# Optimization experiments

Hardware: AMD Instinct MI355X
Metric: run time of the kernel (lower is better)

Reference implementation:

```python
import jax, jax.numpy as jnp
import numpy as np

B, L, D, T, NL = 64, 512, 512, 5000, 2


def setup_inputs() -> dict:
    key = jax.random.key(0)
    k1, k2, k3, k4 = jax.random.split(key, 4)
    enc_output = jax.random.normal(k1, (B, L, D), dtype=jnp.float32)
    # stands in for the row/col-normalized tag co-occurrence matrix (values in [0, 0.01])
    ui_adj = jax.random.uniform(k2, (T, T), dtype=jnp.float32) * 0.01
    # one GCN weight matrix per layer in the layer_stack
    Ws = jax.random.normal(k3, (NL, D, D), dtype=jnp.float32) / np.sqrt(D).astype(np.float32)
    # event ids are 1-indexed in the original (it indexes with e - 1)
    event_type = jax.random.randint(k4, (B, L), 1, T + 1, dtype=jnp.int64)
    slf_attn_mask = jnp.zeros((B, L, L), dtype=bool)
    non_pad_mask = jnp.ones((B, L), dtype=bool)
    return {"enc_output": enc_output, "ui_adj": ui_adj, "Ws": Ws,
            "event_type": event_type, "slf_attn_mask": slf_attn_mask,
            "non_pad_mask": non_pad_mask}


def reference(enc_output, ui_adj, Ws, event_type, slf_attn_mask, non_pad_mask):
    # --- batched per-sample adjacency gather (replaces the Python loop) ---
    idx = event_type - 1                                   # [B, L] 0-indexed
    sub = ui_adj[idx[:, :, None], idx[:, None, :]]         # [B, L, L] = ui_adj[e-1,:][:, e-1]
    diag = ui_adj[idx, idx]                                # [B, L]   = ui_adj[e-1, e-1]
    adj = sub + diag[:, None, :]                           # vector broadcasts across rows, as in torch
    # --- GNN layer stack (hGCN layer ~ relu(A @ X @ W)) ---
    x = enc_output
    for l in range(Ws.shape[0]):                           # small fixed n_layers loop
        x = jax.nn.relu(jnp.einsum('bij,bjd->bid', adj, x) @ Ws[l])
    # --- mean pool over sequence ---
    return x.mean(axis=1)                                  # [B, D]
```

## Files before the change

### kernel.cpp

```cpp
#include <hip/hip_runtime.h>

typedef unsigned short u16;
typedef unsigned int u32;
typedef __bf16 bf16x8 __attribute__((ext_vector_type(8)));
typedef float f32x4 __attribute__((ext_vector_type(4)));
typedef int i32x4 __attribute__((ext_vector_type(4)));
typedef u32 u32x2 __attribute__((ext_vector_type(2)));
typedef u32 u32x4 __attribute__((ext_vector_type(4)));

#define T_ 5000
#define CAP 96

__device__ __forceinline__ u16 f2bf(float f) {
  u32 u = __float_as_uint(f);
  u += 0x7fffu + ((u >> 16) & 1u);
  return (u16)(u >> 16);
}

__device__ __forceinline__ void gload_lds16(const u16* g, u16* l) {
  __builtin_amdgcn_global_load_lds(
      (__attribute__((address_space(1))) void*)(u16*)g,
      (__attribute__((address_space(3))) void*)l, 16, 0, 0);
}

__device__ __forceinline__ u32 lds_off(const void* p) {
  return (u32)(uintptr_t)(__attribute__((address_space(3))) const void*)p;
}

__device__ __forceinline__ u32 swz(int row, int kb) {
  return (u32)((row >> 1) * 128 +
               ((((row & 1) << 6) | kb) ^ (((row >> 1) & 7) << 4)));
}

__global__ void prep_k(const float* __restrict__ src, u16* __restrict__ dst,
                       int* __restrict__ cnt) {
  __shared__ float tile[32][33];
  const int tx = threadIdx.x, ty = threadIdx.y;
  const int a0 = blockIdx.x * 32;
  const int b0 = blockIdx.y * 32;
  const size_t zoff = (size_t)blockIdx.z * (512 * 512);
  const float* s = src + zoff;
  u16* d = dst + zoff;
#pragma unroll
  for (int r = 0; r < 4; ++r)
    tile[ty + r * 8][tx] = s[(size_t)(a0 + ty + r * 8) * 512 + b0 + tx];
  const int gid = ((blockIdx.z * 16 + blockIdx.y) * 16 + blockIdx.x) * 256 + ty * 32 + tx;
  if (gid < 5008) cnt[gid] = 0;
  __syncthreads();
#pragma unroll
  for (int r = 0; r < 4; ++r)
    d[(size_t)(b0 + ty + r * 8) * 512 + a0 + tx] = f2bf(tile[tx][ty + r * 8]);
}

__global__ void fill_k(const int* __restrict__ ev, const float* __restrict__ ui,
                       int2* __restrict__ cd, int* __restrict__ cnt,
                       int* __restrict__ list, int* __restrict__ ovf) {
  const int t = blockIdx.x * 256 + threadIdx.x;
  const int r = ev[t] - 1;
  int2 v;
  v.x = r;
  v.y = __float_as_int(ui[(size_t)r * (T_ + 1)]);
  cd[t] = v;
  const int pos = atomicAdd(&cnt[r], 1);
  if (pos < CAP) list[r * CAP + pos] = t;
  else { const int o = atomicAdd(&cnt[5000], 1); ovf[o] = t; }
}

__global__ __launch_bounds__(256)
void grow_gather(const float* __restrict__ ui, const int2* __restrict__ cd,
                 const int* __restrict__ cnt, const int* __restrict__ list,
                 const int* __restrict__ ovf, u16* __restrict__ adj) {
  __shared__ float row[5000];
  __shared__ int lst[CAP];
  const int r = blockIdx.x;
  int c = cnt[r];
  if (c > CAP) c = CAP;
  const int j = threadIdx.x * 2;
  if (c > 0) {
    const float* __restrict__ src = ui + (size_t)r * T_;
    for (int t = threadIdx.x; t < 1250; t += 256)
      *(float4*)&row[t * 4] = *(const float4*)&src[t * 4];
    if (threadIdx.x < c) lst[threadIdx.x] = list[r * CAP + threadIdx.x];
    __syncthreads();
    int q = 0;
    for (; q + 4 <= c; q += 4) {
      const int t0 = lst[q], t1 = lst[q + 1], t2 = lst[q + 2], t3 = lst[q + 3];
      const int4 p0 = *(const int4*)&cd[((t0 >> 9) << 9) + j];
      const int4 p1 = *(const int4*)&cd[((t1 >> 9) << 9) + j];
      const int4 p2 = *(const int4*)&cd[((t2 >> 9) << 9) + j];
      const int4 p3 = *(const int4*)&cd[((t3 >> 9) << 9) + j];
      const u32 k0 = (u32)f2bf(row[p0.x] + __int_as_float(p0.y)) |
                     ((u32)f2bf(row[p0.z] + __int_as_float(p0.w)) << 16);
      const u32 k1 = (u32)f2bf(row[p1.x] + __int_as_float(p1.y)) |
                     ((u32)f2bf(row[p1.z] + __int_as_float(p1.w)) << 16);
      const u32 k2 = (u32)f2bf(row[p2.x] + __int_as_float(p2.y)) |
                     ((u32)f2bf(row[p2.z] + __int_as_float(p2.w)) << 16);
      const u32 k3 = (u32)f2bf(row[p3.x] + __int_as_float(p3.y)) |
                     ((u32)f2bf(row[p3.z] + __int_as_float(p3.w)) << 16);
      *(u32*)&adj[(size_t)t0 * 512 + j] = k0;
      *(u32*)&adj[(size_t)t1 * 512 + j] = k1;
      *(u32*)&adj[(size_t)t2 * 512 + j] = k2;
      *(u32*)&adj[(size_t)t3 * 512 + j] = k3;
    }
    for (; q < c; ++q) {
      const int t0 = lst[q];
      const int4 p0 = *(const int4*)&cd[((t0 >> 9) << 9) + j];
      const u32 k0 = (u32)f2bf(row[p0.x] + __int_as_float(p0.y)) |
                     ((u32)f2bf(row[p0.z] + __int_as_float(p0.w)) << 16);
      *(u32*)&adj[(size_t)t0 * 512 + j] = k0;
    }
  }
  if (r < 8) {
    const int n = cnt[5000];
    for (int q = r; q < n; q += 8) {
      const int t = ovf[q];
      const long rr = (long)cd[t].x;
      const float* __restrict__ rp = ui + rr * (long)T_;
      const int4 p = *(const int4*)&cd[((t >> 9) << 9) + j];
      const u32 pk = (u32)f2bf(rp[p.x] + __int_as_float(p.y)) |
                     ((u32)f2bf(rp[p.z] + __int_as_float(p.w)) << 16);
      *(u32*)&adj[(size_t)t * 512 + j] = pk;
    }
  }
}

template <int MODE, int BSRC>
__global__ __launch_bounds__(512, 2)
void gemm256(const u16* __restrict__ A, const void* __restrict__ Bv,
             u16* __restrict__ C, size_t strideA, size_t strideB, size_t strideC,
             float* __restrict__ P) {
  extern __shared__ u16 smem[];
  const int tid = threadIdx.x;
  const int lane = tid & 63;
  const int w = tid >> 6;
  const int wm = w >> 2, wn = w & 3;
  const int chunk = gridDim.x >> 3;
  const int wg = blockIdx.x;
  const int mapped = (wg & 7) * chunk + (wg >> 3);
  const int batch = mapped >> 2;
  const int tm = (mapped >> 1) & 1, tn = mapped & 1;
  const int m0 = tm << 8, n0 = tn << 8;
  const int r0base = (MODE == 3) ? n0 : m0;
  const int r1base = (MODE == 3) ? m0 : n0;
  const u16* __restrict__ Ab = A + (size_t)batch * strideA;

  const u16* gA[2];
  u32 ldA[2];
#pragma unroll
  for (int r = 0; r < 2; ++r) {
    const int c = r * 512 + tid;
    const int L = c * 16;
    const int pp = L >> 7;
    const int off = (L & 127) ^ ((pp & 7) << 4);
    const int m = pp * 2 + (off >> 6);
    const int kb = off & 63;
    gA[r] = Ab + (size_t)(r0base + m) * 512 + (kb >> 1);
    ldA[r] = (u32)((r * 512 + w * 64) * 8);
  }

  const u16* gB[2] = {nullptr, nullptr};
  u32 ldB[2] = {0, 0};
  if (BSRC == 0) {
    const u16* __restrict__ Bb = (const u16*)Bv + (size_t)batch * strideB;
#pragma unroll
    for (int r = 0; r < 2; ++r) {
      const int c = r * 512 + tid;
      const int L = c * 16;
      const int pp = L >> 7;
      const int off = (L & 127) ^ ((pp & 7) << 4);
      const int m = pp * 2 + (off >> 6);
      const int kb = off & 63;
      gB[r] = Bb + (size_t)(r1base + m) * 512 + (kb >> 1);
      ldB[r] = (u32)(32768 + (r * 512 + w * 64) * 8);
    }
  }

  const int dp = tid & 127;
  const int lq = tid >> 7;
  unsigned long long encB = 0;
  u32 boff0 = 0;
  u32x2 bs0[8], bs1[8];
  if (BSRC == 1) {
    encB = (unsigned long long)(uintptr_t)((const float*)Bv + (size_t)batch * strideB);
    boff0 = (u32)(((lq * 8) * 512 + r1base + dp * 2) * 4);
  }

#define BLOAD(t, S)                                                          \
  {                                                                          \
    const u32 ob = boff0 + (u32)(t) * 65536u;                                \
    _Pragma("unroll") for (int i = 0; i < 8; ++i)                            \
        asm volatile("global_load_dwordx2 %0, %1, %2"                        \
                     : "=v"(S[i])                                            \
                     : "v"(ob + (u32)i * 2048u), "s"(encB));                 \
  }

#define CONVERT_B(S)                                                         \
  {                                                                          \
    u32 wrd0[4], wrd1[4];                                                    \
    _Pragma("unroll") for (int jj = 0; jj < 4; ++jj) {                       \
      asm("v_cvt_pk_bf16_f32 %0, %1, %2"                                     \
          : "=v"(wrd0[jj]) : "v"(S[2 * jj].x), "v"(S[2 * jj + 1].x));        \
      asm("v_cvt_pk_bf16_f32 %0, %1, %2"                                     \
          : "=v"(wrd1[jj]) : "v"(S[2 * jj].y), "v"(S[2 * jj + 1].y));        \
    }                                                                        \
    const u32 by0 = (u32)dp * 128u + ((((u32)lq * 16u)) ^ (((u32)dp & 7u) << 4)); \
    const u32 by1 = (u32)dp * 128u + ((64u | ((u32)lq * 16u)) ^ (((u32)dp & 7u) << 4)); \
    u32x4 v0, v1;                                                            \
    v0.x = wrd0[0]; v0.y = wrd0[1]; v0.z = wrd0[2]; v0.w = wrd0[3];          \
    v1.x = wrd1[0]; v1.y = wrd1[1]; v1.z = wrd1[2]; v1.w = wrd1[3];          \
    *(u32x4*)((char*)smem + 65536 + by0) = v0;                               \
    *(u32x4*)((char*)smem + 65536 + by1) = v1;                               \
  }

  const int lr = lane & 15;
  const int kbB = (lane >> 4) << 4;
  u32 fOff8[8], fOff4[4];
#pragma unroll
  for (int m = 0; m < 8; ++m) fOff8[m] = swz(wm * 128 + m * 16 + lr, kbB);
#pragma unroll
  for (int n = 0; n < 4; ++n) fOff4[n] = swz(wn * 64 + n * 16 + lr, kbB);
  const u32 ldsBase = lds_off(smem);

  f32x4 acc[8][4] = {};

  auto stageA = [&](int t) {
    const u32 bo = (u32)(t & 3) * 8192;
#pragma unroll
    for (int r = 0; r < 2; ++r) gload_lds16(gA[r] + t * 32, smem + bo + ldA[r]);
  };
  auto stageB0 = [&](int t) {
    const u32 bo = (u32)(t & 3) * 8192;
#pragma unroll
    for (int r = 0; r < 2; ++r) gload_lds16(gB[r] + t * 32, smem + bo + ldB[r]);
  };

  if (BSRC == 0) {
    stageA(0); stageB0(0); stageA(1); stageB0(1); stageA(2); stageB0(2);
  } else {
    stageA(0); stageA(1); stageA(2);
    BLOAD(0, bs0); BLOAD(1, bs1);
  }

#pragma unroll
  for (int t = 0; t < 16; ++t) {
    if (BSRC == 0) {
      if (t <= 13)      asm volatile("s_waitcnt vmcnt(8)" ::: "memory");
      else if (t == 14) asm volatile("s_waitcnt vmcnt(4)" ::: "memory");
      else              asm volatile("s_waitcnt vmcnt(0)" ::: "memory");
      __builtin_amdgcn_sched_barrier(0);
      if (t + 3 < 16) { stageA(t + 3); stageB0(t + 3); }
      asm volatile("" ::: "memory");
      __builtin_amdgcn_s_barrier();
      asm volatile("" ::: "memory");
    } else {
      if (t == 0)              asm volatile("s_waitcnt vmcnt(8)" ::: "memory");
      else if (t <= 13)        asm volatile("s_waitcnt vmcnt(10)" ::: "memory");
      else if (t == 14)        asm volatile("s_waitcnt vmcnt(8)" ::: "memory");
      else                     asm volatile("s_waitcnt vmcnt(0)" ::: "memory");
      __builtin_amdgcn_sched_barrier(0);
      if (t & 1) { CONVERT_B(bs1); } else { CONVERT_B(bs0); }
      if (t + 3 < 16) stageA(t + 3);
      if (t + 2 < 16) { if (t & 1) { BLOAD(t + 2, bs1); } else { BLOAD(t + 2, bs0); } }
      asm volatile("s_waitcnt lgkmcnt(0)" ::: "memory");
      __builtin_amdgcn_s_barrier();
      asm volatile("" ::: "memory");
    }

    const u32 c0 = ldsBase + (u32)(t & 3) * 16384;
    const u32 c1 = ldsBase + 65536u + (BSRC == 0 ? (u32)(t & 3) * 16384 : 0u);
    const u32 base8 = (MODE == 3) ? c1 : c0;
    const u32 base4 = (MODE == 3) ? c0 : c1;
    i32x4 araw[8], braw[4];

#pragma unroll
    for (int n = 0; n < 4; ++n)
      asm volatile("ds_read_b128 %0, %1" : "=v"(braw[n]) : "v"(base4 + fOff4[n]));
#pragma unroll
    for (int m = 0; m < 4; ++m)
      asm volatile("ds_read_b128 %0, %1" : "=v"(araw[m]) : "v"(base8 + fOff8[m]));
    asm volatile("s_waitcnt lgkmcnt(0)" ::: "memory");
    __builtin_amdgcn_sched_barrier(0);
    __builtin_amdgcn_s_setprio(1);
#pragma unroll
    for (int m = 0; m < 4; ++m)
#pragma unroll
      for (int n = 0; n < 4; ++n)
        acc[m][n] = __builtin_amdgcn_mfma_f32_16x16x32_bf16(
            __builtin_bit_cast(bf16x8, araw[m]),
            __builtin_bit_cast(bf16x8, braw[n]), acc[m][n], 0, 0, 0);
    __builtin_amdgcn_s_setprio(0);
    asm volatile("" ::: "memory");
    __builtin_amdgcn_s_barrier();
    asm volatile("" ::: "memory");

#pragma unroll
    for (int m = 4; m < 8; ++m)
      asm volatile("ds_read_b128 %0, %1" : "=v"(araw[m]) : "v"(base8 + fOff8[m]));
    asm volatile("s_waitcnt lgkmcnt(0)" ::: "memory");
    __builtin_amdgcn_sched_barrier(0);
    __builtin_amdgcn_s_setprio(1);
#pragma unroll
    for (int m = 4; m < 8; ++m)
#pragma unroll
      for (int n = 0; n < 4; ++n)
        acc[m][n] = __builtin_amdgcn_mfma_f32_16x16x32_bf16(
            __builtin_bit_cast(bf16x8, araw[m]),
            __builtin_bit_cast(bf16x8, braw[n]), acc[m][n], 0, 0, 0);
    __builtin_amdgcn_s_setprio(0);
    asm volatile("" ::: "memory");
    __builtin_amdgcn_s_barrier();
    __builtin_amdgcn_sched_barrier(0);
  }
#undef BLOAD
#undef CONVERT_B

  u16* Cb = C + (size_t)batch * strideC;
  if (MODE == 1) {
#pragma unroll
    for (int m = 0; m < 8; ++m) {
      const int i = m0 + wm * 128 + m * 16 + (lane >> 4) * 4;
#pragma unroll
      for (int n = 0; n < 4; ++n) {
        const int d = n0 + wn * 64 + n * 16 + (lane & 15);
        const f32x4 v = acc[m][n];
        uint2 p;
        p.x = (u32)f2bf(fmaxf(v[0], 0.f)) | ((u32)f2bf(fmaxf(v[1], 0.f)) << 16);
        p.y = (u32)f2bf(fmaxf(v[2], 0.f)) | ((u32)f2bf(fmaxf(v[3], 0.f)) << 16);
        *(uint2*)&Cb[(size_t)d * 512 + i] = p;
      }
    }
  } else if (MODE == 2) {
    const int slot = tm * 2 + wm;
#pragma unroll
    for (int n = 0; n < 4; ++n) {
      float s = 0.f;
#pragma unroll
      for (int m = 0; m < 8; ++m) {
        const f32x4 v = acc[m][n];
#pragma unroll
        for (int j = 0; j < 4; ++j) s += fmaxf(v[j], 0.f);
      }
      s += __shfl_xor(s, 16);
      s += __shfl_xor(s, 32);
      if ((lane >> 4) == 0) {
        const int d = n0 + wn * 64 + n * 16 + lane;
        P[((size_t)batch * 4 + slot) * 512 + d] = s;
      }
    }
  } else {
#pragma unroll
    for (int m = 0; m < 8; ++m) {
      const int dd = m0 + wm * 128 + m * 16 + (lane >> 4) * 4;
#pragma unroll
      for (int n = 0; n < 4; ++n) {
        const int ii = n0 + wn * 64 + n * 16 + (lane & 15);
        const f32x4 v = acc[m][n];
        uint2 p;
        p.x = (u32)f2bf(v[0]) | ((u32)f2bf(v[1]) << 16);
        p.y = (u32)f2bf(v[2]) | ((u32)f2bf(v[3]) << 16);
        *(uint2*)&Cb[(size_t)ii * 512 + dd] = p;
      }
    }
  }
}

__global__ void reduce_mean(const float* __restrict__ P, float* __restrict__ out) {
  const int t = blockIdx.x * 256 + threadIdx.x;
  const int b = t >> 9, d = t & 511;
  float s = 0.f;
#pragma unroll
  for (int q = 0; q < 4; ++q) s += P[((size_t)b * 4 + q) * 512 + d];
  out[t] = s * (1.0f / 512.0f);
}

extern "C" void kernel_launch(void* const* d_in, const int* in_sizes, int n_in,
                              void* d_out, int out_size, void* d_ws, size_t ws_size,
                              hipStream_t stream) {
  const float* enc = (const float*)d_in[0];
  const float* ui  = (const float*)d_in[1];
  const float* Ws  = (const float*)d_in[2];
  const int*   ev  = (const int*)d_in[3];
  float* out = (float*)d_out;

  char* ws = (char*)d_ws;
  const size_t SLAB = (size_t)64 * 512 * 512 * 2;
  u16* adj  = (u16*)(ws);
  u16* tbuf = (u16*)(ws + SLAB);
  u16* xb   = (u16*)(ws + 2 * SLAB);
  char* p = ws + 3 * SLAB;
  u16* wst  = (u16*)p;  p += (size_t)2 * 512 * 512 * 2;
  int2* cd  = (int2*)p; p += (size_t)32768 * 8;
  int* cnt  = (int*)p;  p += 5008 * 4;
  int* list = (int*)p;  p += (size_t)5000 * CAP * 4;
  int* ovf  = (int*)p;  p += (size_t)32768 * 4;
  float* P  = (float*)p;

  const size_t PS = (size_t)512 * 512;
  const size_t SMEM0 = 131072;
  const size_t SMEM1 = 81920;
  (void)hipFuncSetAttribute(reinterpret_cast<const void*>(gemm256<3, 1>),
                            hipFuncAttributeMaxDynamicSharedMemorySize, (int)SMEM1);
  (void)hipFuncSetAttribute(reinterpret_cast<const void*>(gemm256<1, 0>),
                            hipFuncAttributeMaxDynamicSharedMemorySize, (int)SMEM0);
  (void)hipFuncSetAttribute(reinterpret_cast<const void*>(gemm256<3, 0>),
                            hipFuncAttributeMaxDynamicSharedMemorySize, (int)SMEM0);
  (void)hipFuncSetAttribute(reinterpret_cast<const void*>(gemm256<2, 0>),
                            hipFuncAttributeMaxDynamicSharedMemorySize, (int)SMEM0);

  prep_k<<<dim3(16, 16, 2), dim3(32, 8), 0, stream>>>(Ws, wst, cnt);
  fill_k<<<128, 256, 0, stream>>>(ev, ui, cd, cnt, list, ovf);
  grow_gather<<<5000, 256, 0, stream>>>(ui, cd, cnt, list, ovf, adj);
  gemm256<3, 1><<<256, 512, SMEM1, stream>>>(adj, enc, tbuf, PS, PS, PS, nullptr);
  gemm256<1, 0><<<256, 512, SMEM0, stream>>>(tbuf, wst, xb, PS, 0, PS, nullptr);
  gemm256<3, 0><<<256, 512, SMEM0, stream>>>(adj, xb, tbuf, PS, PS, PS, nullptr);
  gemm256<2, 0><<<256, 512, SMEM0, stream>>>(tbuf, wst + PS, nullptr, PS, 0, 0, P);
  reduce_mean<<<128, 256, 0, stream>>>(P, out);
}
```

Measured before the change: 143.7 us.

## Add 8-phase ping-pong GEMM kernel with 64-wide K tiles for bf16 GEMMs

```diff
diff --git a/kernel.cpp b/kernel.cpp
--- a/kernel.cpp
+++ b/kernel.cpp
@@ -158,23 +158,6 @@
     ldA[r] = (u32)((r * 512 + w * 64) * 8);
   }
 
-  const u16* gB[2] = {nullptr, nullptr};
-  u32 ldB[2] = {0, 0};
-  if (BSRC == 0) {
-    const u16* __restrict__ Bb = (const u16*)Bv + (size_t)batch * strideB;
-#pragma unroll
-    for (int r = 0; r < 2; ++r) {
-      const int c = r * 512 + tid;
-      const int L = c * 16;
-      const int pp = L >> 7;
-      const int off = (L & 127) ^ ((pp & 7) << 4);
-      const int m = pp * 2 + (off >> 6);
-      const int kb = off & 63;
-      gB[r] = Bb + (size_t)(r1base + m) * 512 + (kb >> 1);
-      ldB[r] = (u32)(32768 + (r * 512 + w * 64) * 8);
-    }
-  }
-
   const int dp = tid & 127;
   const int lq = tid >> 7;
   unsigned long long encB = 0;
@@ -228,61 +211,41 @@
 #pragma unroll
     for (int r = 0; r < 2; ++r) gload_lds16(gA[r] + t * 32, smem + bo + ldA[r]);
   };
-  auto stageB0 = [&](int t) {
-    const u32 bo = (u32)(t & 3) * 8192;
-#pragma unroll
-    for (int r = 0; r < 2; ++r) gload_lds16(gB[r] + t * 32, smem + bo + ldB[r]);
-  };
-
-  if (BSRC == 0) {
-    stageA(0); stageB0(0); stageA(1); stageB0(1); stageA(2); stageB0(2);
-  } else {
-    stageA(0); stageA(1); stageA(2);
-    BLOAD(0, bs0); BLOAD(1, bs1);
-  }
+
+  stageA(0); stageA(1); stageA(2);
+  BLOAD(0, bs0); BLOAD(1, bs1);
 
 #pragma unroll
   for (int t = 0; t < 16; ++t) {
-    if (BSRC == 0) {
-      if (t <= 13)      asm volatile("s_waitcnt vmcnt(8)" ::: "memory");
-      else if (t == 14) asm volatile("s_waitcnt vmcnt(4)" ::: "memory");
-      else              asm volatile("s_waitcnt vmcnt(0)" ::: "memory");
-      __builtin_amdgcn_sched_barrier(0);
-      if (t + 3 < 16) { stageA(t + 3); stageB0(t + 3); }
-      asm volatile("" ::: "memory");
-      __builtin_amdgcn_s_barrier();
-      asm volatile("" ::: "memory");
-    } else {
-      if (t == 0)              asm volatile("s_waitcnt vmcnt(8)" ::: "memory");
-      else if (t <= 13)        asm volatile("s_waitcnt vmcnt(10)" ::: "memory");
-      else if (t == 14)        asm volatile("s_waitcnt vmcnt(8)" ::: "memory");
-      else                     asm volatile("s_waitcnt vmcnt(0)" ::: "memory");
-      __builtin_amdgcn_sched_barrier(0);
-      if (t & 1) { CONVERT_B(bs1); } else { CONVERT_B(bs0); }
-      if (t + 3 < 16) stageA(t + 3);
-      if (t + 2 < 16) { if (t & 1) { BLOAD(t + 2, bs1); } else { BLOAD(t + 2, bs0); } }
-      asm volatile("s_waitcnt lgkmcnt(0)" ::: "memory");
-      __builtin_amdgcn_s_barrier();
-      asm volatile("" ::: "memory");
-    }
+    if (t == 0)              asm volatile("s_waitcnt vmcnt(8)" ::: "memory");
+    else if (t <= 13)        asm volatile("s_waitcnt vmcnt(10)" ::: "memory");
+    else if (t == 14)        asm volatile("s_waitcnt vmcnt(8)" ::: "memory");
+    else                     asm volatile("s_waitcnt vmcnt(0)" ::: "memory");
+    __builtin_amdgcn_sched_barrier(0);
+    if (t & 1) { CONVERT_B(bs1); } else { CONVERT_B(bs0); }
+    if (t + 3 < 16) stageA(t + 3);
+    if (t + 2 < 16) { if (t & 1) { BLOAD(t + 2, bs1); } else { BLOAD(t + 2, bs0); } }
+    asm volatile("s_waitcnt lgkmcnt(0)" ::: "memory");
+    __builtin_amdgcn_s_barrier();
+    asm volatile("" ::: "memory");
 
     const u32 c0 = ldsBase + (u32)(t & 3) * 16384;
-    const u32 c1 = ldsBase + 65536u + (BSRC == 0 ? (u32)(t & 3) * 16384 : 0u);
+    const u32 c1 = ldsBase + 65536u;
     const u32 base8 = (MODE == 3) ? c1 : c0;
     const u32 base4 = (MODE == 3) ? c0 : c1;
     i32x4 araw[8], braw[4];
-
+#pragma unroll
+    for (int m = 0; m < 8; ++m)
+      asm volatile("ds_read_b128 %0, %1" : "=v"(araw[m]) : "v"(base8 + fOff8[m]));
 #pragma unroll
     for (int n = 0; n < 4; ++n)
       asm volatile("ds_read_b128 %0, %1" : "=v"(braw[n]) : "v"(base4 + fOff4[n]));
-#pragma unroll
-    for (int m = 0; m < 4; ++m)
-      asm volatile("ds_read_b128 %0, %1" : "=v"(araw[m]) : "v"(base8 + fOff8[m]));
     asm volatile("s_waitcnt lgkmcnt(0)" ::: "memory");
     __builtin_amdgcn_sched_barrier(0);
+
     __builtin_amdgcn_s_setprio(1);
 #pragma unroll
-    for (int m = 0; m < 4; ++m)
+    for (int m = 0; m < 8; ++m)
 #pragma unroll
       for (int n = 0; n < 4; ++n)
         acc[m][n] = __builtin_amdgcn_mfma_f32_16x16x32_bf16(
@@ -291,28 +254,213 @@
     __builtin_amdgcn_s_setprio(0);
     asm volatile("" ::: "memory");
     __builtin_amdgcn_s_barrier();
-    asm volatile("" ::: "memory");
-
-#pragma unroll
-    for (int m = 4; m < 8; ++m)
-      asm volatile("ds_read_b128 %0, %1" : "=v"(araw[m]) : "v"(base8 + fOff8[m]));
-    asm volatile("s_waitcnt lgkmcnt(0)" ::: "memory");
-    __builtin_amdgcn_sched_barrier(0);
-    __builtin_amdgcn_s_setprio(1);
-#pragma unroll
-    for (int m = 4; m < 8; ++m)
-#pragma unroll
-      for (int n = 0; n < 4; ++n)
-        acc[m][n] = __builtin_amdgcn_mfma_f32_16x16x32_bf16(
-            __builtin_bit_cast(bf16x8, araw[m]),
-            __builtin_bit_cast(bf16x8, braw[n]), acc[m][n], 0, 0, 0);
-    __builtin_amdgcn_s_setprio(0);
-    asm volatile("" ::: "memory");
-    __builtin_amdgcn_s_barrier();
     __builtin_amdgcn_sched_barrier(0);
   }
 #undef BLOAD
 #undef CONVERT_B
+
+  u16* Cb = C + (size_t)batch * strideC;
+#pragma unroll
+  for (int m = 0; m < 8; ++m) {
+    const int dd = m0 + wm * 128 + m * 16 + (lane >> 4) * 4;
+#pragma unroll
+    for (int n = 0; n < 4; ++n) {
+      const int ii = n0 + wn * 64 + n * 16 + (lane & 15);
+      const f32x4 v = acc[m][n];
+      uint2 p;
+      p.x = (u32)f2bf(v[0]) | ((u32)f2bf(v[1]) << 16);
+      p.y = (u32)f2bf(v[2]) | ((u32)f2bf(v[3]) << 16);
+      *(uint2*)&Cb[(size_t)ii * 512 + dd] = p;
+    }
+  }
+  (void)P;
+}
+
+template <int MODE>
+__global__ __launch_bounds__(512, 2)
+void gemm8p(const u16* __restrict__ A, const u16* __restrict__ Bm,
+            u16* __restrict__ C, size_t strideA, size_t strideB, size_t strideC,
+            float* __restrict__ P) {
+  extern __shared__ u16 smem[];
+  const int tid = threadIdx.x;
+  const int lane = tid & 63;
+  const int w = tid >> 6;
+  const int wm = w >> 2, wn = w & 3;
+  const int chunk = gridDim.x >> 3;
+  const int wg = blockIdx.x;
+  const int mapped = (wg & 7) * chunk + (wg >> 3);
+  const int batch = mapped >> 2;
+  const int tm = (mapped >> 1) & 1, tn = mapped & 1;
+  const int m0 = tm << 8, n0 = tn << 8;
+  const int r0base = (MODE == 3) ? n0 : m0;
+  const int r1base = (MODE == 3) ? m0 : n0;
+  const u16* __restrict__ Ab = A + (size_t)batch * strideA;
+  const u16* __restrict__ Bb = Bm + (size_t)batch * strideB;
+
+  const u16* gR0[2];
+  const u16* gR1[2];
+  u32 ldR0[2], ldR1[2];
+#pragma unroll
+  for (int rr = 0; rr < 2; ++rr) {
+    const int cc = rr * 512 + tid;
+    const int row = cc >> 3;
+    const int kb = ((cc & 7) * 16) ^ ((row & 7) << 4);
+    gR0[rr] = Ab + (size_t)(r0base + row) * 512 + (kb >> 1);
+    gR1[rr] = Bb + (size_t)(r1base + row) * 512 + (kb >> 1);
+    ldR0[rr] = (u32)((rr * 512 + w * 64) * 8);
+    ldR1[rr] = (u32)(32768 + (rr * 512 + w * 64) * 8);
+  }
+
+  const int lr = lane & 15;
+  const int hi16 = (lane >> 4) * 16;
+  u32 o8[8][2], o4[4][2];
+#pragma unroll
+  for (int m = 0; m < 8; ++m)
+#pragma unroll
+    for (int kk = 0; kk < 2; ++kk) {
+      const int row = wm * 128 + m * 16 + lr;
+      o8[m][kk] = (u32)(row * 128 + ((kk * 64 + hi16) ^ ((lr & 7) << 4)));
+    }
+#pragma unroll
+  for (int n = 0; n < 4; ++n)
+#pragma unroll
+    for (int kk = 0; kk < 2; ++kk) {
+      const int row = wn * 64 + n * 16 + lr;
+      o4[n][kk] = (u32)(row * 128 + ((kk * 64 + hi16) ^ ((lr & 7) << 4)));
+    }
+  const u32 ldsBase = lds_off(smem);
+
+  f32x4 acc[8][4] = {};
+
+  auto stR0 = [&](int tt, int h) {
+    const u32 bo = (u32)((tt & 1) * 16384 + h * 8192);
+#pragma unroll
+    for (int rr = 0; rr < 2; ++rr)
+      gload_lds16(gR0[rr] + (size_t)h * 65536 + tt * 64, smem + bo + ldR0[rr]);
+  };
+  auto stR1 = [&](int tt, int h) {
+    const u32 bo = (u32)((tt & 1) * 16384 + h * 8192);
+#pragma unroll
+    for (int rr = 0; rr < 2; ++rr)
+      gload_lds16(gR1[rr] + (size_t)h * 65536 + tt * 64, smem + bo + ldR1[rr]);
+  };
+  auto stage8 = [&](int tt, int h) { if (MODE == 3) stR1(tt, h); else stR0(tt, h); };
+  auto stage4 = [&](int tt, int h) { if (MODE == 3) stR0(tt, h); else stR1(tt, h); };
+
+  stage4(0, 0); stage4(0, 1); stage8(0, 0); stage8(0, 1); stage4(1, 0); stage4(1, 1);
+  asm volatile("s_waitcnt vmcnt(4)" ::: "memory");
+  __builtin_amdgcn_sched_barrier(0);
+  __builtin_amdgcn_s_barrier();
+
+#pragma unroll
+  for (int t = 0; t < 8; ++t) {
+    const u32 R0b = ldsBase + (u32)(t & 1) * 32768u;
+    const u32 R1b = ldsBase + 65536u + (u32)(t & 1) * 32768u;
+    const u32 b8 = (MODE == 3) ? R1b : R0b;
+    const u32 b4 = (MODE == 3) ? R0b : R1b;
+    i32x4 ar[4][2], b01[2][2], b23[2][2];
+
+#pragma unroll
+    for (int m = 0; m < 4; ++m)
+#pragma unroll
+      for (int kk = 0; kk < 2; ++kk)
+        asm volatile("ds_read_b128 %0, %1" : "=v"(ar[m][kk]) : "v"(b8 + o8[m][kk]));
+#pragma unroll
+    for (int n = 0; n < 2; ++n)
+#pragma unroll
+      for (int kk = 0; kk < 2; ++kk)
+        asm volatile("ds_read_b128 %0, %1" : "=v"(b01[n][kk]) : "v"(b4 + o4[n][kk]));
+    if (t + 1 < 8) stage8(t + 1, 0);
+    asm volatile("" ::: "memory");
+    __builtin_amdgcn_s_barrier();
+    asm volatile("s_waitcnt lgkmcnt(0)" ::: "memory");
+    __builtin_amdgcn_sched_barrier(0);
+    __builtin_amdgcn_s_setprio(1);
+#pragma unroll
+    for (int kk = 0; kk < 2; ++kk)
+#pragma unroll
+      for (int m = 0; m < 4; ++m)
+#pragma unroll
+        for (int n = 0; n < 2; ++n)
+          acc[m][n] = __builtin_amdgcn_mfma_f32_16x16x32_bf16(
+              __builtin_bit_cast(bf16x8, ar[m][kk]),
+              __builtin_bit_cast(bf16x8, b01[n][kk]), acc[m][n], 0, 0, 0);
+    __builtin_amdgcn_s_setprio(0);
+    asm volatile("" ::: "memory");
+    __builtin_amdgcn_s_barrier();
+    __builtin_amdgcn_sched_barrier(0);
+
+#pragma unroll
+    for (int n = 0; n < 2; ++n)
+#pragma unroll
+      for (int kk = 0; kk < 2; ++kk)
+        asm volatile("ds_read_b128 %0, %1" : "=v"(b23[n][kk]) : "v"(b4 + o4[n + 2][kk]));
+    if (t + 1 < 8) stage8(t + 1, 1);
+    asm volatile("" ::: "memory");
+    __builtin_amdgcn_s_barrier();
+    asm volatile("s_waitcnt lgkmcnt(0)" ::: "memory");
+    __builtin_amdgcn_sched_barrier(0);
+    __builtin_amdgcn_s_setprio(1);
+#pragma unroll
+    for (int kk = 0; kk < 2; ++kk)
+#pragma unroll
+      for (int m = 0; m < 4; ++m)
+#pragma unroll
+        for (int n = 0; n < 2; ++n)
+          acc[m][n + 2] = __builtin_amdgcn_mfma_f32_16x16x32_bf16(
+              __builtin_bit_cast(bf16x8, ar[m][kk]),
+              __builtin_bit_cast(bf16x8, b23[n][kk]), acc[m][n + 2], 0, 0, 0);
+    __builtin_amdgcn_s_setprio(0);
+    asm volatile("" ::: "memory");
+    __builtin_amdgcn_s_barrier();
+    __builtin_amdgcn_sched_barrier(0);
+
+#pragma unroll
+    for (int m = 0; m < 4; ++m)
+#pragma unroll
+      for (int kk = 0; kk < 2; ++kk)
+        asm volatile("ds_read_b128 %0, %1" : "=v"(ar[m][kk]) : "v"(b8 + o8[m + 4][kk]));
+    if (t + 2 < 8) stage4(t + 2, 0);
+    asm volatile("" ::: "memory");
+    __builtin_amdgcn_s_barrier();
+    asm volatile("s_waitcnt lgkmcnt(0)" ::: "memory");
+    __builtin_amdgcn_sched_barrier(0);
+    __builtin_amdgcn_s_setprio(1);
+#pragma unroll
+    for (int kk = 0; kk < 2; ++kk)
+#pragma unroll
+      for (int m = 0; m < 4; ++m)
+#pragma unroll
+        for (int n = 0; n < 2; ++n)
+          acc[m + 4][n + 2] = __builtin_amdgcn_mfma_f32_16x16x32_bf16(
+              __builtin_bit_cast(bf16x8, ar[m][kk]),
+              __builtin_bit_cast(bf16x8, b23[n][kk]), acc[m + 4][n + 2], 0, 0, 0);
+    __builtin_amdgcn_s_setprio(0);
+    asm volatile("" ::: "memory");
+    __builtin_amdgcn_s_barrier();
+    __builtin_amdgcn_sched_barrier(0);
+
+    if (t + 2 < 8) stage4(t + 2, 1);
+    if (t <= 5)      asm volatile("s_waitcnt vmcnt(4)" ::: "memory");
+    else if (t == 6) asm volatile("s_waitcnt vmcnt(0)" ::: "memory");
+    __builtin_amdgcn_sched_barrier(0);
+    asm volatile("" ::: "memory");
+    __builtin_amdgcn_s_barrier();
+    __builtin_amdgcn_s_setprio(1);
+#pragma unroll
+    for (int kk = 0; kk < 2; ++kk)
+#pragma unroll
+      for (int m = 0; m < 4; ++m)
+#pragma unroll
+        for (int n = 0; n < 2; ++n)
+          acc[m + 4][n] = __builtin_amdgcn_mfma_f32_16x16x32_bf16(
+              __builtin_bit_cast(bf16x8, ar[m][kk]),
+              __builtin_bit_cast(bf16x8, b01[n][kk]), acc[m + 4][n], 0, 0, 0);
+    __builtin_amdgcn_s_setprio(0);
+    asm volatile("" ::: "memory");
+    __builtin_amdgcn_s_barrier();
+    __builtin_amdgcn_sched_barrier(0);
+  }
 
   u16* Cb = C + (size_t)batch * strideC;
   if (MODE == 1) {
@@ -396,23 +544,23 @@
   float* P  = (float*)p;
 
   const size_t PS = (size_t)512 * 512;
-  const size_t SMEM0 = 131072;
   const size_t SMEM1 = 81920;
+  const size_t SMEM8 = 131072;
   (void)hipFuncSetAttribute(reinterpret_cast<const void*>(gemm256<3, 1>),
                             hipFuncAttributeMaxDynamicSharedMemorySize, (int)SMEM1);
-  (void)hipFuncSetAttribute(reinterpret_cast<const void*>(gemm256<1, 0>),
-                            hipFuncAttributeMaxDynamicSharedMemorySize, (int)SMEM0);
-  (void)hipFuncSetAttribute(reinterpret_cast<const void*>(gemm256<3, 0>),
-                            hipFuncAttributeMaxDynamicSharedMemorySize, (int)SMEM0);
-  (void)hipFuncSetAttribute(reinterpret_cast<const void*>(gemm256<2, 0>),
-                            hipFuncAttributeMaxDynamicSharedMemorySize, (int)SMEM0);
+  (void)hipFuncSetAttribute(reinterpret_cast<const void*>(gemm8p<1>),
+                            hipFuncAttributeMaxDynamicSharedMemorySize, (int)SMEM8);
+  (void)hipFuncSetAttribute(reinterpret_cast<const void*>(gemm8p<3>),
+                            hipFuncAttributeMaxDynamicSharedMemorySize, (int)SMEM8);
+  (void)hipFuncSetAttribute(reinterpret_cast<const void*>(gemm8p<2>),
+                            hipFuncAttributeMaxDynamicSharedMemorySize, (int)SMEM8);
 
   prep_k<<<dim3(16, 16, 2), dim3(32, 8), 0, stream>>>(Ws, wst, cnt);
   fill_k<<<128, 256, 0, stream>>>(ev, ui, cd, cnt, list, ovf);
   grow_gather<<<5000, 256, 0, stream>>>(ui, cd, cnt, list, ovf, adj);
   gemm256<3, 1><<<256, 512, SMEM1, stream>>>(adj, enc, tbuf, PS, PS, PS, nullptr);
-  gemm256<1, 0><<<256, 512, SMEM0, stream>>>(tbuf, wst, xb, PS, 0, PS, nullptr);
-  gemm256<3, 0><<<256, 512, SMEM0, stream>>>(adj, xb, tbuf, PS, PS, PS, nullptr);
-  gemm256<2, 0><<<256, 512, SMEM0, stream>>>(tbuf, wst + PS, nullptr, PS, 0, 0, P);
+  gemm8p<1><<<256, 512, SMEM8, stream>>>(tbuf, wst, xb, PS, 0, PS, nullptr);
+  gemm8p<3><<<256, 512, SMEM8, stream>>>(adj, xb, tbuf, PS, PS, PS, nullptr);
+  gemm8p<2><<<256, 512, SMEM8, stream>>>(tbuf, wst + PS, nullptr, PS, 0, 0, P);
   reduce_mean<<<128, 256, 0, stream>>>(P, out);
 }
```

Measured after the change: 150.3 us. 1.05x slower.
